# Optimization experiments

Hardware: AMD Instinct MI355X
Metric: run time of the kernel (lower is better)

## Reference

```python
import jax, jax.numpy as jnp
import numpy as np

N, E = 50000, 800000
D_IN, H, D_OUT = 100, 128, 40
N_MID = 2  # num_layers(5) - 3
EPS = 1e-5


def setup_inputs() -> dict:
    key = jax.random.key(0)
    ks = iter(jax.random.split(key, 40))
    rn = lambda shape, s=0.05: jax.random.normal(next(ks), shape, dtype=jnp.float32) * s
    inp = {
        "x": jax.random.normal(next(ks), (N, D_IN), dtype=jnp.float32),
        "edge_index": jax.random.randint(next(ks), (2, E), 0, N, dtype=jnp.int64),
        "percent": 70,
        "ricci_curvature": jax.random.normal(next(ks), (E,), dtype=jnp.float32),
        # GCNConv weights/biases
        "W1": rn((D_IN, H)), "b1": jnp.zeros((H,), jnp.float32),
        "W2": rn((D_IN + H, H)), "b2": jnp.zeros((H,), jnp.float32),
        "Wm": rn((N_MID, 2 * H, H)), "bm": jnp.zeros((N_MID, H), jnp.float32),
        "Wo": rn((2 * H, D_OUT)), "bo": jnp.zeros((D_OUT,), jnp.float32),
    }
    # BatchNorm1d params + running stats (eval mode)
    def bn_params(dim, lead=()):
        return (jnp.ones(lead + (dim,), jnp.float32),            # gamma
                jnp.zeros(lead + (dim,), jnp.float32),           # beta
                rn(lead + (dim,), 0.1),                          # running mean
                1.0 + 0.1 * jax.random.uniform(next(ks), lead + (dim,), dtype=jnp.float32))  # running var
    inp["bn1_g"], inp["bn1_b"], inp["bn1_m"], inp["bn1_v"] = bn_params(D_IN)
    inp["bn2_g"], inp["bn2_b"], inp["bn2_m"], inp["bn2_v"] = bn_params(D_IN + H)
    inp["bnm_g"], inp["bnm_b"], inp["bnm_m"], inp["bnm_v"] = bn_params(2 * H, (N_MID,))
    inp["bno_g"], inp["bno_b"], inp["bno_m"], inp["bno_v"] = bn_params(2 * H)
    return inp


def reference(x, edge_index, percent, ricci_curvature,
              W1, b1, W2, b2, Wm, bm, Wo, bo,
              bn1_g, bn1_b, bn1_m, bn1_v,
              bn2_g, bn2_b, bn2_m, bn2_v,
              bnm_g, bnm_b, bnm_m, bnm_v,
              bno_g, bno_b, bno_m, bno_v):
    # Eval mode: no sampling / dynamic edge weights, dropout = identity,
    # BN uses running stats. GCNConv = PyG: add self-loops, sym-norm D^-1/2 A D^-1/2.
    n = x.shape[0]
    loop = jnp.arange(n)
    src = jnp.concatenate([edge_index[0], loop])  # [E+N]
    dst = jnp.concatenate([edge_index[1], loop])
    deg = jnp.zeros((n,), x.dtype).at[dst].add(1.0)  # >=1 thanks to self-loops
    dis = jax.lax.rsqrt(deg)
    norm = (dis[src] * dis[dst])[:, None]  # [E+N, 1]

    def gcn(h, W, b):
        hw = h @ W  # [N, out]
        agg = jnp.zeros((n, W.shape[1]), h.dtype).at[dst].add(hw[src] * norm)
        return agg + b

    def bn(h, g, bta, m, v):
        return (h - m) * (g * jax.lax.rsqrt(v + EPS)) + bta

    res = []
    x_in = x
    h = jax.nn.relu(gcn(bn(x, bn1_g, bn1_b, bn1_m, bn1_v), W1, b1))
    res.append(h)
    h = jnp.concatenate([h, x_in], axis=1)  # [N, H+D_IN]
    h = jax.nn.relu(gcn(bn(h, bn2_g, bn2_b, bn2_m, bn2_v), W2, b2))
    res.append(h)
    h = jnp.concatenate([h, res[-2]], axis=1)  # [N, 2H]
    for i in range(Wm.shape[0]):
        hi = jax.nn.relu(gcn(bn(h, bnm_g[i], bnm_b[i], bnm_m[i], bnm_v[i]), Wm[i], bm[i]))
        res.append(hi)
        h = jnp.concatenate([hi, res[-2]], axis=1)
    out = gcn(bn(h, bno_g, bno_b, bno_m, bno_v), Wo, bo)
    return (out, *res)
```

## Files before the change

kernel.cpp:

```cpp
#include <hip/hip_runtime.h>
#include <hip/hip_bf16.h>
#include <cstdint>
#include <cstddef>

#define BN_EPS 1e-5f
typedef long long ll;
using bf16x8 = __attribute__((ext_vector_type(8))) short;
using f32x4  = __attribute__((ext_vector_type(4))) float;

__device__ __forceinline__ unsigned short f2bf(float f) {
    union { float f; unsigned u; } c; c.f = f;
    unsigned u = c.u;
    u += 0x7fff + ((u >> 16) & 1);
    return (unsigned short)(u >> 16);
}
__device__ __forceinline__ float bf2f(unsigned h) {
    union { unsigned u; float f; } c; c.u = h << 16;
    return c.f;
}
__device__ __forceinline__ void addbf8(float* a, uint4 v) {
    a[0] += bf2f(v.x & 0xffffu); a[1] += bf2f(v.x >> 16);
    a[2] += bf2f(v.y & 0xffffu); a[3] += bf2f(v.y >> 16);
    a[4] += bf2f(v.z & 0xffffu); a[5] += bf2f(v.z >> 16);
    a[6] += bf2f(v.w & 0xffffu); a[7] += bf2f(v.w >> 16);
}
__device__ __forceinline__ float4 bf4_to_f4(uint2 v) {
    return make_float4(bf2f(v.x & 0xffffu), bf2f(v.x >> 16),
                       bf2f(v.y & 0xffffu), bf2f(v.y >> 16));
}
__device__ __forceinline__ void gload_lds16(const void* g, void* lds) {
    __builtin_amdgcn_global_load_lds(
        (const __attribute__((address_space(1))) unsigned int*)g,
        (__attribute__((address_space(3))) unsigned int*)lds, 16, 0, 0);
}

__global__ void build0_kernel(const int* ei32, int* flag, int* deg, int* cursor, int N) {
    int i = blockIdx.x * 256 + threadIdx.x;
    if (i < N) { deg[i] = 1; cursor[i] = 0; }
    if (blockIdx.x == 0) {
        __shared__ int any;
        if (threadIdx.x == 0) any = 0;
        __syncthreads();
        for (int t = threadIdx.x; t < 2048; t += 256)
            if (ei32[2 * t + 1] != 0) any = 1;
        __syncthreads();
        if (threadIdx.x == 0) *flag = (any == 0) ? 1 : 0;
    }
}

__global__ void count_kernel(const void* ei, int E, int* deg, const int* flag) {
    int e = blockIdx.x * 256 + threadIdx.x;
    if (e >= E) return;
    int d = (*flag) ? (int)((const ll*)ei)[(size_t)E + e]
                    : ((const int*)ei)[(size_t)E + e];
    atomicAdd(&deg[d], 1);
}

__global__ __launch_bounds__(1024) void scanA_kernel(const int* deg, int* row_ptr,
                                                     int* bsum, float* dis, int N) {
    __shared__ int wsum[16];
    int i = blockIdx.x * 1024 + threadIdx.x;
    int lane = threadIdx.x & 63, wid = threadIdx.x >> 6;
    int dv = (i < N) ? deg[i] : 1;
    if (i < N) dis[i] = rsqrtf((float)dv);
    int v = (i < N) ? (dv - 1) : 0;
    int s = v;
#pragma unroll
    for (int o = 1; o < 64; o <<= 1) { int t = __shfl_up(s, o); if (lane >= o) s += t; }
    if (lane == 63) wsum[wid] = s;
    __syncthreads();
    if (threadIdx.x < 16) {
        int w = wsum[threadIdx.x];
        int ws_ = w;
#pragma unroll
        for (int o = 1; o < 16; o <<= 1) { int t = __shfl_up(ws_, o); if ((int)threadIdx.x >= o) ws_ += t; }
        wsum[threadIdx.x] = ws_ - w;
    }
    __syncthreads();
    s += wsum[wid];
    if (i < N) row_ptr[i + 1] = s;
    if (threadIdx.x == 1023) bsum[blockIdx.x] = s;
}

__global__ void scanB_kernel(int* bsum, int nb) {
    int lane = threadIdx.x;
    int v = (lane < nb) ? bsum[lane] : 0;
    int s = v;
#pragma unroll
    for (int o = 1; o < 64; o <<= 1) { int t = __shfl_up(s, o); if (lane >= o) s += t; }
    if (lane < nb) bsum[lane] = s - v;
}

__global__ __launch_bounds__(1024) void scanC_kernel(int* row_ptr, const int* bsum, int N) {
    int i = blockIdx.x * 1024 + threadIdx.x;
    if (i < N) row_ptr[i + 1] += bsum[blockIdx.x];
    if (i == 0) row_ptr[0] = 0;
}

__global__ void fill_kernel(const void* ei, int E, const int* row_ptr,
                            int* cursor, int* csr, const int* flag) {
    int e = blockIdx.x * 256 + threadIdx.x;
    if (e >= E) return;
    int s, d;
    if (*flag) { const ll* p = (const ll*)ei; s = (int)p[e]; d = (int)p[(size_t)E + e]; }
    else       { const int* p = (const int*)ei; s = p[e]; d = p[(size_t)E + e]; }
    int pos = atomicAdd(&cursor[d], 1);
    csr[row_ptr[d] + pos] = s;
}

struct LayerP {
    const float *W, *g, *b, *m, *v;
    int K, Dout, ncb, boff;
};
struct LayerPs { LayerP l[5]; };

__global__ __launch_bounds__(256) void fold_all(LayerPs P,
                                                unsigned short* __restrict__ Bhi,
                                                unsigned short* __restrict__ Blo,
                                                float* __restrict__ cvecA) {
    const LayerP& L = P.l[blockIdx.y];
    if (blockIdx.x < 128) {
        int nkc = (L.K + 63) >> 6 << 1;
        int total = nkc * L.ncb * 512;
        int idx = blockIdx.x * 256 + threadIdx.x;
        if (idx >= total) return;
        int i = idx & 7;
        int lane = (idx >> 3) & 63;
        int cb = (idx >> 9) % L.ncb;
        int kc = (idx >> 9) / L.ncb;
        int k = kc * 32 + (lane >> 4) * 8 + i;
        int col = cb * 16 + (lane & 15);
        float val = 0.f;
        if (k < L.K && col < L.Dout) {
            float s = L.g[k] * rsqrtf(L.v[k] + BN_EPS);
            val = L.W[k * L.Dout + col] * s;
        }
        unsigned short h = f2bf(val);
        Bhi[L.boff + idx] = h;
        Blo[L.boff + idx] = f2bf(val - bf2f(h));
    } else {
        int wid = threadIdx.x >> 6, lane = threadIdx.x & 63;
        int col = (blockIdx.x - 128) * 4 + wid;
        float acc = 0.f;
        if (col < L.Dout) {
            for (int k = lane; k < L.K; k += 64) {
                float s = L.g[k] * rsqrtf(L.v[k] + BN_EPS);
                acc += (L.b[k] - L.m[k] * s) * L.W[k * L.Dout + col];
            }
        }
#pragma unroll
        for (int o = 32; o >= 1; o >>= 1) acc += __shfl_xor(acc, o);
        if (lane == 0 && col < 128) cvecA[128 * blockIdx.y + col] = (col < L.Dout) ? acc : 0.f;
    }
}

__global__ __launch_bounds__(256, 4) void gemm_bf2_kernel(
    const unsigned short* __restrict__ X1, int K1, int ld1,
    const unsigned short* __restrict__ X2, int ld2,
    const unsigned short* __restrict__ Bhi, const unsigned short* __restrict__ Blo,
    const float* __restrict__ cvec, const float* __restrict__ dis,
    unsigned short* __restrict__ outp, int K, int N)
{
    __shared__ unsigned short Xs[64 * 64];
    const int tid = threadIdx.x;
    const int w = tid >> 6, lane = tid & 63;
    const int lr = lane & 15, lg = lane >> 4;
    const int brow = blockIdx.x * 64;
    const int nkt = (K + 63) >> 6;
    const int cb0 = 2 * w;

    f32x4 acc[4][2];
#pragma unroll
    for (int c = 0; c < 2; ++c) {
        float cv = cvec[(cb0 + c) * 16 + lr];
        f32x4 iv = {cv, cv, cv, cv};
#pragma unroll
        for (int rb = 0; rb < 4; ++rb) acc[rb][c] = iv;
    }

    for (int kt = 0; kt < nkt; ++kt) {
        const int k0 = kt * 64;
        const unsigned short* T = (k0 < K1) ? X1 : X2;
        const int ldT = (k0 < K1) ? ld1 : ld2;
        const int kb = (k0 < K1) ? k0 : (k0 - K1);
#pragma unroll
        for (int p = 0; p < 2; ++p) {
            int idx = p * 256 + tid;
            int r = idx >> 3;
            int sl = idx & 7;
            int grow = brow + r; if (grow >= N) grow = N - 1;
            int ksl = sl ^ (r & 7);
            gload_lds16(T + (size_t)grow * ldT + kb + ksl * 8,
                        (char*)Xs + (size_t)(p * 256 + w * 64) * 16);
        }
        __syncthreads();

#pragma unroll
        for (int ks = 0; ks < 2; ++ks) {
            const int kcg = kt * 2 + ks;
            bf16x8 a[4];
#pragma unroll
            for (int rb = 0; rb < 4; ++rb) {
                int r = rb * 16 + lr;
                a[rb] = *(const bf16x8*)((const char*)Xs + r * 128 +
                                         ((ks * 64 + lg * 16) ^ ((r & 7) << 4)));
            }
            const bf16x8* bh = (const bf16x8*)Bhi + (size_t)kcg * 8 * 64;
            const bf16x8* bl = (const bf16x8*)Blo + (size_t)kcg * 8 * 64;
#pragma unroll
            for (int c = 0; c < 2; ++c) {
                bf16x8 bhf = bh[(cb0 + c) * 64 + lane];
                bf16x8 blf = bl[(cb0 + c) * 64 + lane];
#pragma unroll
                for (int rb = 0; rb < 4; ++rb) {
                    acc[rb][c] = __builtin_amdgcn_mfma_f32_16x16x32_bf16(a[rb], bhf, acc[rb][c], 0, 0, 0);
                    acc[rb][c] = __builtin_amdgcn_mfma_f32_16x16x32_bf16(a[rb], blf, acc[rb][c], 0, 0, 0);
                }
            }
        }
        __syncthreads();
    }

#pragma unroll
    for (int rb = 0; rb < 4; ++rb) {
#pragma unroll
        for (int r = 0; r < 4; ++r) {
            int grow = brow + rb * 16 + lg * 4 + r;
            if (grow >= N) continue;
            float d = dis[grow];
#pragma unroll
            for (int c = 0; c < 2; ++c)
                outp[(size_t)grow * 128 + (cb0 + c) * 16 + lr] = f2bf(d * acc[rb][c][r]);
        }
    }
}

template <bool B1, bool B2>
__global__ __launch_bounds__(256, 3) void gemm_mix2_kernel(
    const void* __restrict__ X1, int K1, int ld1,
    const void* __restrict__ X2, int ld2,
    const unsigned short* __restrict__ Bhi, const unsigned short* __restrict__ Blo,
    const float* __restrict__ cvec, const float* __restrict__ dis,
    unsigned short* __restrict__ outp, int K, int kc_lo, int N)
{
    __shared__ unsigned short Xhi[64 * 64];
    __shared__ unsigned short Xlo[64 * 64];
    const int tid = threadIdx.x;
    const int w = tid >> 6, lane = tid & 63;
    const int lr = lane & 15, lg = lane >> 4;
    const int brow = blockIdx.x * 64;
    const int nkt = (K + 63) >> 6;
    const int cb0 = 2 * w;

    f32x4 acc[4][2];
#pragma unroll
    for (int c = 0; c < 2; ++c) {
        float cv = cvec[(cb0 + c) * 16 + lr];
        f32x4 iv = {cv, cv, cv, cv};
#pragma unroll
        for (int rb = 0; rb < 4; ++rb) acc[rb][c] = iv;
    }

    for (int kt = 0; kt < nkt; ++kt) {
        const int k0 = kt * 64;
        const bool kt_lo = (kt * 2 + 1) >= kc_lo;
#pragma unroll
        for (int p = 0; p < 4; ++p) {
            int fidx = (p * 256 + tid) * 4;
            int r = fidx >> 6;
            int c = fidx & 63;
            int grow = brow + r;
            int k = k0 + c;
            float4 val = make_float4(0.f, 0.f, 0.f, 0.f);
            if (grow < N) {
                if (k < K1) {
                    if (B1) val = bf4_to_f4(*(const uint2*)((const unsigned short*)X1 + (size_t)grow * ld1 + k));
                    else    val = *(const float4*)((const float*)X1 + (size_t)grow * ld1 + k);
                } else if (k < K) {
                    int kk = k - K1;
                    if (B2) val = bf4_to_f4(*(const uint2*)((const unsigned short*)X2 + (size_t)grow * ld2 + kk));
                    else    val = *(const float4*)((const float*)X2 + (size_t)grow * ld2 + kk);
                }
            }
            unsigned short h0 = f2bf(val.x), h1 = f2bf(val.y),
                           h2 = f2bf(val.z), h3 = f2bf(val.w);
            int b8 = c * 2;
            int addr = r * 128 + (((b8 & 0x70) ^ ((r & 7) << 4)) | (b8 & 8));
            *(uint2*)((char*)Xhi + addr) =
                make_uint2((unsigned)h0 | ((unsigned)h1 << 16),
                           (unsigned)h2 | ((unsigned)h3 << 16));
            if (kt_lo) {
                unsigned short l0 = f2bf(val.x - bf2f(h0)), l1 = f2bf(val.y - bf2f(h1)),
                               l2 = f2bf(val.z - bf2f(h2)), l3 = f2bf(val.w - bf2f(h3));
                *(uint2*)((char*)Xlo + addr) =
                    make_uint2((unsigned)l0 | ((unsigned)l1 << 16),
                               (unsigned)l2 | ((unsigned)l3 << 16));
            }
        }
        __syncthreads();

#pragma unroll
        for (int ks = 0; ks < 2; ++ks) {
            const int kcg = kt * 2 + ks;
            const bool need_lo = (kcg >= kc_lo);
            bf16x8 ah[4], al[4];
#pragma unroll
            for (int rb = 0; rb < 4; ++rb) {
                int r = rb * 16 + lr;
                int off = ((ks * 64 + lg * 16) ^ ((r & 7) << 4));
                ah[rb] = *(const bf16x8*)((const char*)Xhi + r * 128 + off);
                if (need_lo) al[rb] = *(const bf16x8*)((const char*)Xlo + r * 128 + off);
            }
            const bf16x8* bh = (const bf16x8*)Bhi + (size_t)kcg * 8 * 64;
            const bf16x8* bl = (const bf16x8*)Blo + (size_t)kcg * 8 * 64;
#pragma unroll
            for (int c = 0; c < 2; ++c) {
                bf16x8 bhf = bh[(cb0 + c) * 64 + lane];
                bf16x8 blf = bl[(cb0 + c) * 64 + lane];
#pragma unroll
                for (int rb = 0; rb < 4; ++rb) {
                    acc[rb][c] = __builtin_amdgcn_mfma_f32_16x16x32_bf16(ah[rb], bhf, acc[rb][c], 0, 0, 0);
                    acc[rb][c] = __builtin_amdgcn_mfma_f32_16x16x32_bf16(ah[rb], blf, acc[rb][c], 0, 0, 0);
                    if (need_lo)
                        acc[rb][c] = __builtin_amdgcn_mfma_f32_16x16x32_bf16(al[rb], bhf, acc[rb][c], 0, 0, 0);
                }
            }
        }
        __syncthreads();
    }

#pragma unroll
    for (int rb = 0; rb < 4; ++rb) {
#pragma unroll
        for (int r = 0; r < 4; ++r) {
            int grow = brow + rb * 16 + lg * 4 + r;
            if (grow >= N) continue;
            float d = dis[grow];
#pragma unroll
            for (int c = 0; c < 2; ++c)
                outp[(size_t)grow * 128 + (cb0 + c) * 16 + lr] = f2bf(d * acc[rb][c][r]);
        }
    }
}

__global__ __launch_bounds__(256, 4) void gemm_bf40_kernel(
    const unsigned short* __restrict__ X1, int K1, int ld1,
    const unsigned short* __restrict__ X2, int ld2,
    const unsigned short* __restrict__ Bhi, const unsigned short* __restrict__ Blo,
    const float* __restrict__ cvec, const float* __restrict__ dis,
    unsigned short* __restrict__ outp, int K, int N)
{
    __shared__ unsigned short Xs[64 * 64];
    const int tid = threadIdx.x;
    const int w = tid >> 6, lane = tid & 63;
    const int lr = lane & 15, lg = lane >> 4;
    const int brow = blockIdx.x * 64;
    const int nkt = (K + 63) >> 6;

    f32x4 acc[3];
#pragma unroll
    for (int cb = 0; cb < 3; ++cb) {
        float cv = cvec[cb * 16 + lr];
        f32x4 iv = {cv, cv, cv, cv};
        acc[cb] = iv;
    }

    for (int kt = 0; kt < nkt; ++kt) {
        const int k0 = kt * 64;
        const unsigned short* T = (k0 < K1) ? X1 : X2;
        const int ldT = (k0 < K1) ? ld1 : ld2;
        const int kb = (k0 < K1) ? k0 : (k0 - K1);
#pragma unroll
        for (int p = 0; p < 2; ++p) {
            int idx = p * 256 + tid;
            int r = idx >> 3;
            int sl = idx & 7;
            int grow = brow + r; if (grow >= N) grow = N - 1;
            int ksl = sl ^ (r & 7);
            gload_lds16(T + (size_t)grow * ldT + kb + ksl * 8,
                        (char*)Xs + (size_t)(p * 256 + w * 64) * 16);
        }
        __syncthreads();

        const int r = w * 16 + lr;
        const char* base = (const char*)Xs + r * 128;
        const int swz = (r & 7) << 4;
        bf16x8 a0 = *(const bf16x8*)(base + ((lg * 16) ^ swz));
        bf16x8 a1 = *(const bf16x8*)(base + ((64 + lg * 16) ^ swz));
#pragma unroll
        for (int ks = 0; ks < 2; ++ks) {
            const int kcg = kt * 2 + ks;
            const bf16x8 af = ks ? a1 : a0;
            const bf16x8* bh = (const bf16x8*)Bhi + (size_t)kcg * 3 * 64;
            const bf16x8* bl = (const bf16x8*)Blo + (size_t)kcg * 3 * 64;
#pragma unroll
            for (int cb = 0; cb < 3; ++cb) {
                bf16x8 bhf = bh[cb * 64 + lane];
                bf16x8 blf = bl[cb * 64 + lane];
                acc[cb] = __builtin_amdgcn_mfma_f32_16x16x32_bf16(af, bhf, acc[cb], 0, 0, 0);
                acc[cb] = __builtin_amdgcn_mfma_f32_16x16x32_bf16(af, blf, acc[cb], 0, 0, 0);
            }
        }
        __syncthreads();
    }

#pragma unroll
    for (int r = 0; r < 4; ++r) {
        int grow = brow + w * 16 + lg * 4 + r;
        if (grow >= N) continue;
        float d = dis[grow];
#pragma unroll
        for (int cb = 0; cb < 3; ++cb) {
            int col = cb * 16 + lr;
            if (col < 40) outp[(size_t)grow * 40 + col] = f2bf(d * acc[cb][r]);
        }
    }
}

template <bool RELU>
__global__ __launch_bounds__(256) void agg128b_kernel(
    const unsigned short* __restrict__ hwb,
    const int* __restrict__ row_ptr, const int* __restrict__ csr,
    const float* __restrict__ dis, const float* __restrict__ bias,
    float* __restrict__ outp, unsigned short* __restrict__ hbout, int N)
{
    int wid = threadIdx.x >> 6, lane = threadIdx.x & 63;
    int node = blockIdx.x * 4 + wid;
    if (node >= N) return;
    const int sg = lane >> 4, q = lane & 15;
    const uint4* hw4 = (const uint4*)hwb;
    float a[8] = {0.f, 0.f, 0.f, 0.f, 0.f, 0.f, 0.f, 0.f};
    float b8[8] = {0.f, 0.f, 0.f, 0.f, 0.f, 0.f, 0.f, 0.f};
    if (sg == 0) addbf8(a, hw4[(size_t)node * 16 + q]);
    int beg = row_ptr[node], end = row_ptr[node + 1];
    for (int base = beg; base < end; base += 64) {
        int idx = base + lane;
        int j = (idx < end) ? csr[idx] : 0;
        int cnt = end - base; if (cnt > 64) cnt = 64;
        int fullq = cnt >> 2;
        int t = 0;
        for (; t + 2 <= fullq; t += 2) {
            int ja = __shfl(j, 4 * t + sg);
            int jb = __shfl(j, 4 * t + 4 + sg);
            uint4 va = hw4[(size_t)ja * 16 + q];
            uint4 vb = hw4[(size_t)jb * 16 + q];
            addbf8(a, va); addbf8(b8, vb);
        }
        for (; t < fullq; ++t) {
            int ja = __shfl(j, 4 * t + sg);
            uint4 va = hw4[(size_t)ja * 16 + q];
            addbf8(a, va);
        }
        int rem = cnt & 3;
        if (rem) {
            int srcl = (cnt & ~3) + ((sg < rem) ? sg : 0);
            int ja = __shfl(j, srcl);
            if (sg < rem) {
                uint4 va = hw4[(size_t)ja * 16 + q];
                addbf8(a, va);
            }
        }
    }
#pragma unroll
    for (int c = 0; c < 8; ++c) {
        a[c] += b8[c];
        a[c] += __shfl_xor(a[c], 16);
        a[c] += __shfl_xor(a[c], 32);
    }
    if (sg == 0) {
        float d = dis[node];
        float4 bv0 = ((const float4*)bias)[q * 2];
        float4 bv1 = ((const float4*)bias)[q * 2 + 1];
        float o[8];
        o[0] = fmaf(d, a[0], bv0.x); o[1] = fmaf(d, a[1], bv0.y);
        o[2] = fmaf(d, a[2], bv0.z); o[3] = fmaf(d, a[3], bv0.w);
        o[4] = fmaf(d, a[4], bv1.x); o[5] = fmaf(d, a[5], bv1.y);
        o[6] = fmaf(d, a[6], bv1.z); o[7] = fmaf(d, a[7], bv1.w);
        if (RELU) {
#pragma unroll
            for (int c = 0; c < 8; ++c) o[c] = fmaxf(o[c], 0.f);
        }
        ((float4*)outp)[(size_t)node * 32 + q * 2]     = make_float4(o[0], o[1], o[2], o[3]);
        ((float4*)outp)[(size_t)node * 32 + q * 2 + 1] = make_float4(o[4], o[5], o[6], o[7]);
        uint4 pk;
        pk.x = (unsigned)f2bf(o[0]) | ((unsigned)f2bf(o[1]) << 16);
        pk.y = (unsigned)f2bf(o[2]) | ((unsigned)f2bf(o[3]) << 16);
        pk.z = (unsigned)f2bf(o[4]) | ((unsigned)f2bf(o[5]) << 16);
        pk.w = (unsigned)f2bf(o[6]) | ((unsigned)f2bf(o[7]) << 16);
        ((uint4*)hbout)[(size_t)node * 16 + q] = pk;
    }
}

__global__ __launch_bounds__(256) void agg40b_kernel(
    const unsigned short* __restrict__ hwb,
    const int* __restrict__ row_ptr, const int* __restrict__ csr,
    const float* __restrict__ dis, const float* __restrict__ bias,
    float* __restrict__ outp, int N)
{
    int wid = threadIdx.x >> 6, lane = threadIdx.x & 63;
    int node = blockIdx.x * 4 + wid;
    if (node >= N) return;
    const int half = lane >> 5, q = lane & 31;
    const bool act = q < 20;
    const unsigned* hw20 = (const unsigned*)hwb;
    float a0 = 0.f, a1 = 0.f, b0 = 0.f, b1 = 0.f;
    if (half == 0 && act) {
        unsigned v = hw20[(size_t)node * 20 + q];
        a0 += bf2f(v & 0xffffu); a1 += bf2f(v >> 16);
    }
    int beg = row_ptr[node], end = row_ptr[node + 1];
    for (int base = beg; base < end; base += 64) {
        int idx = base + lane;
        int j = (idx < end) ? csr[idx] : 0;
        int cnt = end - base; if (cnt > 64) cnt = 64;
        int fullp = cnt >> 1;
        int t = 0;
        for (; t + 4 <= fullp; t += 4) {
            int ja = __shfl(j, 2 * t     + half);
            int jb = __shfl(j, 2 * t + 2 + half);
            int jc = __shfl(j, 2 * t + 4 + half);
            int jd = __shfl(j, 2 * t + 6 + half);
            if (act) {
                unsigned va = hw20[(size_t)ja * 20 + q];
                unsigned vb = hw20[(size_t)jb * 20 + q];
                unsigned vc = hw20[(size_t)jc * 20 + q];
                unsigned vd = hw20[(size_t)jd * 20 + q];
                a0 += bf2f(va & 0xffffu); a1 += bf2f(va >> 16);
                b0 += bf2f(vb & 0xffffu); b1 += bf2f(vb >> 16);
                a0 += bf2f(vc & 0xffffu); a1 += bf2f(vc >> 16);
                b0 += bf2f(vd & 0xffffu); b1 += bf2f(vd >> 16);
            }
        }
        for (; t < fullp; ++t) {
            int ja = __shfl(j, 2 * t + half);
            if (act) {
                unsigned va = hw20[(size_t)ja * 20 + q];
                a0 += bf2f(va & 0xffffu); a1 += bf2f(va >> 16);
            }
        }
        if (cnt & 1) {
            int ja = __shfl(j, cnt - 1);
            if (half == 0 && act) {
                unsigned va = hw20[(size_t)ja * 20 + q];
                a0 += bf2f(va & 0xffffu); a1 += bf2f(va >> 16);
            }
        }
    }
    a0 += b0; a1 += b1;
    a0 += __shfl_xor(a0, 32);
    a1 += __shfl_xor(a1, 32);
    if (half == 0 && act) {
        float d = dis[node];
        float2 o;
        o.x = fmaf(d, a0, bias[2 * q]);
        o.y = fmaf(d, a1, bias[2 * q + 1]);
        *(float2*)(outp + (size_t)node * 40 + 2 * q) = o;
    }
}

extern "C" void kernel_launch(void* const* d_in, const int* in_sizes, int n_in,
                              void* d_out, int out_size, void* d_ws, size_t ws_size,
                              hipStream_t stream) {
    const int N = in_sizes[0] / 100;
    const int E = in_sizes[1] / 2;

    const float* x   = (const float*)d_in[0];
    const void*  ei  = d_in[1];
    const float* W1  = (const float*)d_in[4];
    const float* b1  = (const float*)d_in[5];
    const float* W2  = (const float*)d_in[6];
    const float* b2  = (const float*)d_in[7];
    const float* Wm  = (const float*)d_in[8];
    const float* bm  = (const float*)d_in[9];
    const float* Wo  = (const float*)d_in[10];
    const float* bo  = (const float*)d_in[11];
    const float* bn1g = (const float*)d_in[12];
    const float* bn1b = (const float*)d_in[13];
    const float* bn1m = (const float*)d_in[14];
    const float* bn1v = (const float*)d_in[15];
    const float* bn2g = (const float*)d_in[16];
    const float* bn2b = (const float*)d_in[17];
    const float* bn2m = (const float*)d_in[18];
    const float* bn2v = (const float*)d_in[19];
    const float* bnmg = (const float*)d_in[20];
    const float* bnmb = (const float*)d_in[21];
    const float* bnmm = (const float*)d_in[22];
    const float* bnmv = (const float*)d_in[23];
    const float* bnog = (const float*)d_in[24];
    const float* bnob = (const float*)d_in[25];
    const float* bnom = (const float*)d_in[26];
    const float* bnov = (const float*)d_in[27];

    char* wsb = (char*)d_ws;
    size_t off = 0;
    auto alloc = [&](size_t elems) -> void* { void* p = wsb + off; off += elems * 4; return p; };
    int*   deg     = (int*)alloc(N);
    int*   cursor  = (int*)alloc(N);
    int*   row_ptr = (int*)alloc((size_t)N + 1);
    int*   bsum    = (int*)alloc(64);
    int*   flag    = (int*)alloc(1);
    off = (off + 15) & ~(size_t)15;
    float* dis  = (float*)alloc(N);
    int*   csr  = (int*)alloc(E);
    off = (off + 15) & ~(size_t)15;
    unsigned short* hwb = (unsigned short*)alloc((size_t)N * 64);
    unsigned short* hbA = (unsigned short*)alloc((size_t)N * 64);
    unsigned short* hbB = (unsigned short*)alloc((size_t)N * 64);
    unsigned short* hbC = (unsigned short*)alloc((size_t)N * 64);
    unsigned short* BhiA = (unsigned short*)alloc(63488);
    unsigned short* BloA = (unsigned short*)alloc(63488);
    float* cvecA = (float*)alloc(128 * 5);
    (void)ws_size; (void)n_in; (void)out_size;

    float* outF = (float*)d_out;
    float* h1 = outF + (size_t)N * 40;
    float* h2 = h1 + (size_t)N * 128;
    float* h3 = h2 + (size_t)N * 128;
    float* h4 = h3 + (size_t)N * 128;

    dim3 b256(256);

    LayerPs P;
    P.l[0] = {W1, bn1g, bn1b, bn1m, bn1v, 100, 128, 8, 0};
    P.l[1] = {W2, bn2g, bn2b, bn2m, bn2v, 228, 128, 8, 16384};
    P.l[2] = {Wm, bnmg, bnmb, bnmm, bnmv, 256, 128, 8, 49152};
    P.l[3] = {Wm + 256 * 128, bnmg + 256, bnmb + 256, bnmm + 256, bnmv + 256, 256, 128, 8, 81920};
    P.l[4] = {Wo, bnog, bnob, bnom, bnov, 256, 40, 3, 114688};
    fold_all<<<dim3(160, 5), b256, 0, stream>>>(P, BhiA, BloA, cvecA);

    build0_kernel<<<dim3((N + 255) / 256), b256, 0, stream>>>((const int*)ei, flag, deg, cursor, N);
    count_kernel<<<dim3((E + 255) / 256), b256, 0, stream>>>(ei, E, deg, flag);
    int nb = (N + 1023) / 1024;
    scanA_kernel<<<dim3(nb), dim3(1024), 0, stream>>>(deg, row_ptr, bsum, dis, N);
    scanB_kernel<<<1, 64, 0, stream>>>(bsum, nb);
    scanC_kernel<<<dim3(nb), dim3(1024), 0, stream>>>(row_ptr, bsum, N);
    fill_kernel<<<dim3((E + 255) / 256), b256, 0, stream>>>(ei, E, row_ptr, cursor, csr, flag);

    int gemm_grid = (N + 63) / 64;
    int agg_grid  = (N + 3) / 4;

    auto agg128 = [&](const float* lb, float* dst, unsigned short* hbout) {
        agg128b_kernel<true><<<dim3(agg_grid), b256, 0, stream>>>(
            hwb, row_ptr, csr, dis, lb, dst, hbout, N);
    };

    gemm_mix2_kernel<false, false><<<dim3(gemm_grid), b256, 0, stream>>>(
        x, 100, 100, nullptr, 0, BhiA + P.l[0].boff, BloA + P.l[0].boff,
        cvecA, dis, hwb, 100, 0, N);
    agg128(b1, h1, hbA);

    gemm_mix2_kernel<true, false><<<dim3(gemm_grid), b256, 0, stream>>>(
        hbA, 128, 128, x, 100, BhiA + P.l[1].boff, BloA + P.l[1].boff,
        cvecA + 128, dis, hwb, 228, 4, N);
    agg128(b2, h2, hbB);

    gemm_bf2_kernel<<<dim3(gemm_grid), b256, 0, stream>>>(
        hbB, 128, 128, hbA, 128, BhiA + P.l[2].boff, BloA + P.l[2].boff,
        cvecA + 256, dis, hwb, 256, N);
    agg128(bm, h3, hbC);

    gemm_bf2_kernel<<<dim3(gemm_grid), b256, 0, stream>>>(
        hbC, 128, 128, hbB, 128, BhiA + P.l[3].boff, BloA + P.l[3].boff,
        cvecA + 384, dis, hwb, 256, N);
    agg128(bm + 128, h4, hbA);

    gemm_bf40_kernel<<<dim3(gemm_grid), b256, 0, stream>>>(
        hbA, 128, 128, hbC, 128, BhiA + P.l[4].boff, BloA + P.l[4].boff,
        cvecA + 512, dis, hwb, 256, N);
    agg40b_kernel<<<dim3(agg_grid), b256, 0, stream>>>(hwb, row_ptr, csr, dis, bo, outF, N);
}
```

Measured before the change: 387.7 us.

## Double-buffer LDS tiles in bf2 and bf40 GEMM kernels to overlap loads

```diff
diff --git a/kernel.cpp b/kernel.cpp
--- a/kernel.cpp
+++ b/kernel.cpp
@@ -161,7 +161,7 @@
     const float* __restrict__ cvec, const float* __restrict__ dis,
     unsigned short* __restrict__ outp, int K, int N)
 {
-    __shared__ unsigned short Xs[64 * 64];
+    __shared__ unsigned short Xs[2][64 * 64];
     const int tid = threadIdx.x;
     const int w = tid >> 6, lane = tid & 63;
     const int lr = lane & 15, lg = lane >> 4;
@@ -169,31 +169,46 @@
     const int nkt = (K + 63) >> 6;
     const int cb0 = 2 * w;
 
-    f32x4 acc[4][2];
-#pragma unroll
-    for (int c = 0; c < 2; ++c) {
-        float cv = cvec[(cb0 + c) * 16 + lr];
-        f32x4 iv = {cv, cv, cv, cv};
-#pragma unroll
-        for (int rb = 0; rb < 4; ++rb) acc[rb][c] = iv;
-    }
-
-    for (int kt = 0; kt < nkt; ++kt) {
+    int s_r[2], s_sl[2];
+#pragma unroll
+    for (int p = 0; p < 2; ++p) {
+        int idx = p * 256 + tid;
+        s_r[p] = idx >> 3;
+        s_sl[p] = idx & 7;
+    }
+
+    auto STAGE = [&](int kt, int b) {
         const int k0 = kt * 64;
         const unsigned short* T = (k0 < K1) ? X1 : X2;
         const int ldT = (k0 < K1) ? ld1 : ld2;
         const int kb = (k0 < K1) ? k0 : (k0 - K1);
 #pragma unroll
         for (int p = 0; p < 2; ++p) {
-            int idx = p * 256 + tid;
-            int r = idx >> 3;
-            int sl = idx & 7;
-            int grow = brow + r; if (grow >= N) grow = N - 1;
-            int ksl = sl ^ (r & 7);
+            int grow = brow + s_r[p]; if (grow >= N) grow = N - 1;
+            int ksl = s_sl[p] ^ (s_r[p] & 7);
             gload_lds16(T + (size_t)grow * ldT + kb + ksl * 8,
-                        (char*)Xs + (size_t)(p * 256 + w * 64) * 16);
-        }
-        __syncthreads();
+                        (char*)Xs[b] + (size_t)(p * 256 + w * 64) * 16);
+        }
+    };
+
+    f32x4 acc[4][2];
+#pragma unroll
+    for (int c = 0; c < 2; ++c) {
+        float cv = cvec[(cb0 + c) * 16 + lr];
+        f32x4 iv = {cv, cv, cv, cv};
+#pragma unroll
+        for (int rb = 0; rb < 4; ++rb) acc[rb][c] = iv;
+    }
+
+    STAGE(0, 0);
+    for (int kt = 0; kt < nkt; ++kt) {
+        const int cur = kt & 1;
+        if (kt + 1 < nkt) STAGE(kt + 1, cur ^ 1);
+        __builtin_amdgcn_sched_barrier(0);
+        if (kt + 1 < nkt) asm volatile("s_waitcnt vmcnt(2)" ::: "memory");
+        else              asm volatile("s_waitcnt vmcnt(0)" ::: "memory");
+        __builtin_amdgcn_s_barrier();
+        __builtin_amdgcn_sched_barrier(0);
 
 #pragma unroll
         for (int ks = 0; ks < 2; ++ks) {
@@ -202,7 +217,7 @@
 #pragma unroll
             for (int rb = 0; rb < 4; ++rb) {
                 int r = rb * 16 + lr;
-                a[rb] = *(const bf16x8*)((const char*)Xs + r * 128 +
+                a[rb] = *(const bf16x8*)((const char*)Xs[cur] + r * 128 +
                                          ((ks * 64 + lg * 16) ^ ((r & 7) << 4)));
             }
             const bf16x8* bh = (const bf16x8*)Bhi + (size_t)kcg * 8 * 64;
@@ -218,7 +233,9 @@
                 }
             }
         }
-        __syncthreads();
+        asm volatile("s_waitcnt lgkmcnt(0)" ::: "memory");
+        __builtin_amdgcn_s_barrier();
+        __builtin_amdgcn_sched_barrier(0);
     }
 
 #pragma unroll
@@ -350,13 +367,34 @@
     const float* __restrict__ cvec, const float* __restrict__ dis,
     unsigned short* __restrict__ outp, int K, int N)
 {
-    __shared__ unsigned short Xs[64 * 64];
+    __shared__ unsigned short Xs[2][64 * 64];
     const int tid = threadIdx.x;
     const int w = tid >> 6, lane = tid & 63;
     const int lr = lane & 15, lg = lane >> 4;
     const int brow = blockIdx.x * 64;
     const int nkt = (K + 63) >> 6;
 
+    int s_r[2], s_sl[2];
+#pragma unroll
+    for (int p = 0; p < 2; ++p) {
+        int idx = p * 256 + tid;
+        s_r[p] = idx >> 3;
+        s_sl[p] = idx & 7;
+    }
+    auto STAGE = [&](int kt, int b) {
+        const int k0 = kt * 64;
+        const unsigned short* T = (k0 < K1) ? X1 : X2;
+        const int ldT = (k0 < K1) ? ld1 : ld2;
+        const int kb = (k0 < K1) ? k0 : (k0 - K1);
+#pragma unroll
+        for (int p = 0; p < 2; ++p) {
+            int grow = brow + s_r[p]; if (grow >= N) grow = N - 1;
+            int ksl = s_sl[p] ^ (s_r[p] & 7);
+            gload_lds16(T + (size_t)grow * ldT + kb + ksl * 8,
+                        (char*)Xs[b] + (size_t)(p * 256 + w * 64) * 16);
+        }
+    };
+
     f32x4 acc[3];
 #pragma unroll
     for (int cb = 0; cb < 3; ++cb) {
@@ -365,25 +403,18 @@
         acc[cb] = iv;
     }
 
+    STAGE(0, 0);
     for (int kt = 0; kt < nkt; ++kt) {
-        const int k0 = kt * 64;
-        const unsigned short* T = (k0 < K1) ? X1 : X2;
-        const int ldT = (k0 < K1) ? ld1 : ld2;
-        const int kb = (k0 < K1) ? k0 : (k0 - K1);
-#pragma unroll
-        for (int p = 0; p < 2; ++p) {
-            int idx = p * 256 + tid;
-            int r = idx >> 3;
-            int sl = idx & 7;
-            int grow = brow + r; if (grow >= N) grow = N - 1;
-            int ksl = sl ^ (r & 7);
-            gload_lds16(T + (size_t)grow * ldT + kb + ksl * 8,
-                        (char*)Xs + (size_t)(p * 256 + w * 64) * 16);
-        }
-        __syncthreads();
+        const int cur = kt & 1;
+        if (kt + 1 < nkt) STAGE(kt + 1, cur ^ 1);
+        __builtin_amdgcn_sched_barrier(0);
+        if (kt + 1 < nkt) asm volatile("s_waitcnt vmcnt(2)" ::: "memory");
+        else              asm volatile("s_waitcnt vmcnt(0)" ::: "memory");
+        __builtin_amdgcn_s_barrier();
+        __builtin_amdgcn_sched_barrier(0);
 
         const int r = w * 16 + lr;
-        const char* base = (const char*)Xs + r * 128;
+        const char* base = (const char*)Xs[cur] + r * 128;
         const int swz = (r & 7) << 4;
         bf16x8 a0 = *(const bf16x8*)(base + ((lg * 16) ^ swz));
         bf16x8 a1 = *(const bf16x8*)(base + ((64 + lg * 16) ^ swz));
@@ -401,7 +432,9 @@
                 acc[cb] = __builtin_amdgcn_mfma_f32_16x16x32_bf16(af, blf, acc[cb], 0, 0, 0);
             }
         }
-        __syncthreads();
+        asm volatile("s_waitcnt lgkmcnt(0)" ::: "memory");
+        __builtin_amdgcn_s_barrier();
+        __builtin_amdgcn_sched_barrier(0);
     }
 
 #pragma unroll
```

Result: faster. 378.1 us, median of 2 (-2.5%).
